# Kernel optimization log

Hardware: AMD Instinct MI355X
Metric: run time of the kernel (lower is better)

## Reference

```python
import jax, jax.numpy as jnp
import numpy as np

B = 256
# (Cin, Cout, K, Hout) for each of the 6 deformable conv layers; input is 33x33
_LAYERS = [(1, 16, 3, 31), (16, 32, 3, 29), (32, 16, 5, 25), (16, 16, 7, 19), (16, 8, 5, 15), (8, 4, 3, 13)]


def setup_inputs() -> dict:
    key = jax.random.key(0)
    ks = jax.random.split(key, 24)
    inp = {"x": jax.random.normal(ks[0], (B, 1, 33, 33), dtype=jnp.float32)}
    for i, (ci, co, k, ho) in enumerate(_LAYERS):
        inp[f"off{i+1}"] = jax.random.normal(ks[1 + i], (1, 2 * k * k, ho, ho), dtype=jnp.float32)
        inp[f"w{i+1}"] = jax.random.normal(ks[7 + i], (co, ci, k, k), dtype=jnp.float32) / float(np.sqrt(ci * k * k))
        inp[f"b{i+1}"] = jnp.zeros((co,), jnp.float32)
    inp["w7"] = jax.random.normal(ks[13], (13 * 13 * 4, 256), dtype=jnp.float32) / 26.0
    inp["b7"] = jnp.zeros((256,), jnp.float32)
    inp["w8"] = jax.random.normal(ks[14], (256, 10), dtype=jnp.float32) / 16.0
    inp["b8"] = jnp.zeros((10,), jnp.float32)
    inp["perm"] = jnp.arange(13 * 13, dtype=jnp.int32)  # fixed spatial permutation (perm_6.ordenar)
    return inp


def _deform_conv(x, offset, weight, bias):
    # torchvision DeformConv2d, stride=1, padding=0, fixed offsets shared across batch.
    Bn, Cin, H, W = x.shape
    Cout, _, K, _ = weight.shape
    Ho, Wo = offset.shape[-2], offset.shape[-1]
    K2 = K * K
    off = offset[0].reshape(K2, 2, Ho, Wo)  # channel layout: [2k]=dy, [2k+1]=dx
    ky, kx = jnp.meshgrid(jnp.arange(K), jnp.arange(K), indexing='ij')
    py = jnp.arange(Ho, dtype=x.dtype)[None, :, None] + ky.reshape(-1, 1, 1) + off[:, 0]  # [K2,Ho,Wo]
    px = jnp.arange(Wo, dtype=x.dtype)[None, None, :] + kx.reshape(-1, 1, 1) + off[:, 1]
    y0f = jnp.floor(py); x0f = jnp.floor(px)
    wy = py - y0f; wx = px - x0f
    y0 = y0f.astype(jnp.int32); x0 = x0f.astype(jnp.int32)
    xf = x.reshape(Bn, Cin, H * W)

    def gather(yi, xi):
        valid = ((yi >= 0) & (yi < H) & (xi >= 0) & (xi < W)).astype(x.dtype)
        idx = (jnp.clip(yi, 0, H - 1) * W + jnp.clip(xi, 0, W - 1)).reshape(-1)
        v = xf[:, :, idx].reshape(Bn, Cin, K2, Ho, Wo)
        return v * valid[None, None]

    s = (gather(y0, x0) * ((1 - wy) * (1 - wx))[None, None]
         + gather(y0, x0 + 1) * ((1 - wy) * wx)[None, None]
         + gather(y0 + 1, x0) * (wy * (1 - wx))[None, None]
         + gather(y0 + 1, x0 + 1) * (wy * wx)[None, None])  # [B,Cin,K2,Ho,Wo]
    out = jnp.einsum('bckhw,ock->bohw', s, weight.reshape(Cout, Cin, K2))
    return out + bias[None, :, None, None]


def reference(x, off1, off2, off3, off4, off5, off6,
              w1, b1, w2, b2, w3, b3, w4, b4, w5, b5, w6, b6,
              w7, b7, w8, b8, perm):
    offs = (off1, off2, off3, off4, off5, off6)
    ws = (w1, w2, w3, w4, w5, w6)
    bs = (b1, b2, b3, b4, b5, b6)
    for off, w, b in zip(offs, ws, bs):
        x = jax.nn.relu(_deform_conv(x, off, w, b))
    Bn = x.shape[0]
    x = x.reshape(Bn, 4, 13 * 13)[:, :, perm].reshape(Bn, -1)  # perm_6.ordenar as spatial permutation
    h = jax.nn.relu(x @ w7 + b7)
    return h @ w8 + b8
```

## Files before the change

### kernel.cpp

```cpp
#include <hip/hip_runtime.h>

struct WtArgs { const float* src[6]; int co[6], ci[6], k2[6], dstoff[6]; };

__global__ __launch_bounds__(256)
void transpose_weights(WtArgs a, float* __restrict__ dst0)
{
    const int L = blockIdx.x;
    const float* __restrict__ s = a.src[L];
    float* __restrict__ d = dst0 + a.dstoff[L];
    const int co = a.co[L], ci = a.ci[L], k2 = a.k2[L];
    const int n = co * ci * k2;
    for (int i = threadIdx.x; i < n; i += 256) {
        int k = i % k2;
        int c = (i / k2) % ci;
        int o = i / (k2 * ci);
        d[(k * ci + c) * co + o] = s[i];
    }
}

struct MetaArgs { const float* off[6]; int P[6], K[6], WO[6], H[6], W[6], base[6]; };

__global__ __launch_bounds__(256)
void build_meta(MetaArgs a, float* __restrict__ meta0)
{
    const int L = blockIdx.y;
    const float* __restrict__ off = a.off[L];
    const int P = a.P[L], K = a.K[L], WOv = a.WO[L], H = a.H[L], Wv = a.W[L];
    const int N = P * K * K;
    float* __restrict__ m = meta0 + (size_t)a.base[L] * 8;
    for (int e = blockIdx.x * 256 + threadIdx.x; e < N; e += gridDim.x * 256) {
        const int k = e / P, p = e - k * P;
        const int ho = p / WOv, wo = p - ho * WOv;
        const int ky = k / K, kx = k - ky * K;
        const float dy = off[(2 * k)     * P + p];
        const float dx = off[(2 * k + 1) * P + p];
        const float py = (float)(ho + ky) + dy;
        const float px = (float)(wo + kx) + dx;
        const float y0f = floorf(py), x0f = floorf(px);
        const float wy = py - y0f, wx = px - x0f;
        const int y0 = (int)y0f, x0 = (int)x0f;
        const int y1 = y0 + 1,  x1 = x0 + 1;
        const bool vy0 = ((unsigned)y0 < (unsigned)H);
        const bool vy1 = ((unsigned)y1 < (unsigned)H);
        const bool vx0 = ((unsigned)x0 < (unsigned)Wv);
        const bool vx1 = ((unsigned)x1 < (unsigned)Wv);
        const int cy0 = min(max(y0, 0), H - 1) * Wv;
        const int cy1 = min(max(y1, 0), H - 1) * Wv;
        const int cx0 = min(max(x0, 0), Wv - 1);
        const int cx1 = min(max(x1, 0), Wv - 1);
        int4 mi;
        mi.x = cy0 + cx0; mi.y = cy0 + cx1; mi.z = cy1 + cx0; mi.w = cy1 + cx1;
        float4 mw;
        mw.x = (vy0 && vx0) ? (1.f - wy) * (1.f - wx) : 0.f;
        mw.y = (vy0 && vx1) ? (1.f - wy) * wx         : 0.f;
        mw.z = (vy1 && vx0) ? wy * (1.f - wx)         : 0.f;
        mw.w = (vy1 && vx1) ? wy * wx                 : 0.f;
        *(int4*)(m + (size_t)e * 8)     = mi;
        *(float4*)(m + (size_t)e * 8 + 4) = mw;
    }
}

template<int CIN, int CINW, int COUT, int K, int H, int W, int HO, int WO,
         int S, int KSEG, int NT, int NCOMB, bool SPLITOUT, bool MET>
__global__ __launch_bounds__(NT)
void deform_lds(const float* __restrict__ x0, const float* __restrict__ x1,
                const float* __restrict__ off, const float* __restrict__ meta,
                const float* __restrict__ wT, const float* __restrict__ bias,
                float* __restrict__ y, size_t pstride)
{
    constexpr int K2 = K * K, HW = H * W, P = HO * WO;
    constexpr int PW = ((P + 63) / 64) * 64;
    constexpr int KLEN = (K2 + KSEG - 1) / KSEG;
    constexpr int PSTR = (COUT % 2 == 0) ? COUT + 1 : COUT;
    static_assert(NT >= KSEG * PW, "NT too small for KSEG*PW");

    __shared__ __align__(16) float simg[HW * S];
    __shared__ float part[(KSEG > 1) ? (KSEG - 1) * P * PSTR : 1];

    const int tid = threadIdx.x;
    const int b   = blockIdx.x;
    const int h   = SPLITOUT ? blockIdx.y : 0;

    const size_t xoff = (size_t)b * CINW * HW + (SPLITOUT ? (size_t)h * CIN * HW : 0);
    const float* xb  = x0 + xoff;
    const float* xb1 = (NCOMB == 2) ? (x1 + xoff) : nullptr;
    for (int i = tid; i < CIN * HW; i += NT) {
        int c = i / HW, hw = i - c * HW;
        float v;
        if constexpr (NCOMB == 2) v = fmaxf(xb[i] + xb1[i], 0.f);
        else                      v = xb[i];
        simg[hw * S + c] = v;
    }
    __syncthreads();

    const int g  = tid / PW;
    const int p  = tid - g * PW;
    const int pc = (p < P) ? p : (P - 1);
    const bool active = (p < P);

    float acc[COUT];
#pragma unroll
    for (int o = 0; o < COUT; ++o) acc[o] = 0.f;

    if (g < KSEG) {
        if (g == 0 && (!SPLITOUT || h == 0)) {
#pragma unroll
            for (int o = 0; o < COUT; ++o) acc[o] = bias[o];
        }
        const int ho = pc / WO, wo = pc - ho * WO;
        const int kb = g * KLEN;

        auto fma_block = [&](int i00, int i01, int i10, int i11,
                             float w00, float w01, float w10, float w11,
                             int kku) {
            const float* __restrict__ r00 = simg + i00 * S;
            const float* __restrict__ r01 = simg + i01 * S;
            const float* __restrict__ r10 = simg + i10 * S;
            const float* __restrict__ r11 = simg + i11 * S;
            const float* __restrict__ wk = wT + kku * (CINW * COUT)
                                         + (SPLITOUT ? h * (CIN * COUT) : 0);
            if constexpr (CIN % 4 == 0) {
#pragma unroll
                for (int c4 = 0; c4 < CIN / 4; ++c4) {
                    const float4 v00 = *(const float4*)(r00 + c4 * 4);
                    const float4 v01 = *(const float4*)(r01 + c4 * 4);
                    const float4 v10 = *(const float4*)(r10 + c4 * 4);
                    const float4 v11 = *(const float4*)(r11 + c4 * 4);
                    float4 sa;
                    sa.x = fmaf(w00, v00.x, fmaf(w01, v01.x, fmaf(w10, v10.x, w11 * v11.x)));
                    sa.y = fmaf(w00, v00.y, fmaf(w01, v01.y, fmaf(w10, v10.y, w11 * v11.y)));
                    sa.z = fmaf(w00, v00.z, fmaf(w01, v01.z, fmaf(w10, v10.z, w11 * v11.z)));
                    sa.w = fmaf(w00, v00.w, fmaf(w01, v01.w, fmaf(w10, v10.w, w11 * v11.w)));
                    const float* __restrict__ wc = wk + (c4 * 4) * COUT;
#pragma unroll
                    for (int o = 0; o < COUT; ++o) acc[o] = fmaf(wc[o], sa.x, acc[o]);
#pragma unroll
                    for (int o = 0; o < COUT; ++o) acc[o] = fmaf(wc[COUT + o], sa.y, acc[o]);
#pragma unroll
                    for (int o = 0; o < COUT; ++o) acc[o] = fmaf(wc[2 * COUT + o], sa.z, acc[o]);
#pragma unroll
                    for (int o = 0; o < COUT; ++o) acc[o] = fmaf(wc[3 * COUT + o], sa.w, acc[o]);
                }
            } else {
#pragma unroll
                for (int c = 0; c < CIN; ++c) {
                    float sa = fmaf(w00, r00[c], fmaf(w01, r01[c],
                               fmaf(w10, r10[c], w11 * r11[c])));
#pragma unroll
                    for (int o = 0; o < COUT; ++o)
                        acc[o] = fmaf(wk[c * COUT + o], sa, acc[o]);
                }
            }
        };

        if constexpr (MET) {
            const int kf = (kb < K2) ? kb : (K2 - 1);
            int4   nmi = *(const int4*)  (meta + (size_t)(kf * P + pc) * 8);
            float4 nmw = *(const float4*)(meta + (size_t)(kf * P + pc) * 8 + 4);

#pragma unroll 1
            for (int j = 0; j < KLEN; ++j) {
                const int k  = kb + j;
                const int kk = (k < K2) ? k : (K2 - 1);
                const int4   mi  = nmi;
                const float4 mwv = nmw;
                const int kn = (k + 1 < K2) ? (k + 1) : (K2 - 1);
                nmi = *(const int4*)  (meta + (size_t)(kn * P + pc) * 8);
                nmw = *(const float4*)(meta + (size_t)(kn * P + pc) * 8 + 4);

                float w00 = mwv.x, w01 = mwv.y, w10 = mwv.z, w11 = mwv.w;
                if constexpr (K2 % KSEG != 0) {
                    const float kv = (k < K2) ? 1.f : 0.f;
                    w00 *= kv; w01 *= kv; w10 *= kv; w11 *= kv;
                }
                const int kku = __builtin_amdgcn_readfirstlane(kk);
                fma_block(mi.x, mi.y, mi.z, mi.w, w00, w01, w10, w11, kku);
            }
        } else {
            const int kf = (kb < K2) ? kb : (K2 - 1);
            float ndy = off[(2 * kf)     * P + pc];
            float ndx = off[(2 * kf + 1) * P + pc];

#pragma unroll 1
            for (int j = 0; j < KLEN; ++j) {
                const int k  = kb + j;
                const int kk = (k < K2) ? k : (K2 - 1);
                const float dy = ndy, dx = ndx;
                const int kn = (k + 1 < K2) ? (k + 1) : (K2 - 1);
                ndy = off[(2 * kn)     * P + pc];
                ndx = off[(2 * kn + 1) * P + pc];

                const int ky = kk / K, kx = kk - ky * K;
                const float py = (float)(ho + ky) + dy;
                const float px = (float)(wo + kx) + dx;
                const float y0f = floorf(py), x0f = floorf(px);
                const float wy = py - y0f, wx = px - x0f;
                const int y0 = (int)y0f, x0 = (int)x0f;
                const int y1 = y0 + 1,  x1i = x0 + 1;
                const bool vy0 = ((unsigned)y0  < (unsigned)H);
                const bool vy1 = ((unsigned)y1  < (unsigned)H);
                const bool vx0 = ((unsigned)x0  < (unsigned)W);
                const bool vx1 = ((unsigned)x1i < (unsigned)W);
                const int cy0 = min(max(y0, 0), H - 1) * W;
                const int cy1 = min(max(y1, 0), H - 1) * W;
                const int cx0 = min(max(x0, 0), W - 1);
                const int cx1 = min(max(x1i, 0), W - 1);
                float w00 = (vy0 && vx0) ? (1.f - wy) * (1.f - wx) : 0.f;
                float w01 = (vy0 && vx1) ? (1.f - wy) * wx         : 0.f;
                float w10 = (vy1 && vx0) ? wy * (1.f - wx)         : 0.f;
                float w11 = (vy1 && vx1) ? wy * wx                 : 0.f;
                if constexpr (K2 % KSEG != 0) {
                    const float kv = (k < K2) ? 1.f : 0.f;
                    w00 *= kv; w01 *= kv; w10 *= kv; w11 *= kv;
                }
                const int kku = __builtin_amdgcn_readfirstlane(kk);
                fma_block(cy0 + cx0, cy0 + cx1, cy1 + cx0, cy1 + cx1,
                          w00, w01, w10, w11, kku);
            }
        }

        if (g > 0 && active) {
#pragma unroll
            for (int o = 0; o < COUT; ++o)
                part[(g - 1) * (P * PSTR) + p * PSTR + o] = acc[o];
        }
    }

    if constexpr (KSEG > 1) __syncthreads();

    if (g == 0 && active) {
        if constexpr (KSEG > 1) {
#pragma unroll
            for (int gg = 1; gg < KSEG; ++gg)
#pragma unroll
                for (int o = 0; o < COUT; ++o)
                    acc[o] += part[(gg - 1) * (P * PSTR) + p * PSTR + o];
        }
        float* yb = y + (SPLITOUT ? (size_t)h * pstride : 0) + (size_t)b * COUT * P;
#pragma unroll
        for (int o = 0; o < COUT; ++o)
            yb[o * P + p] = SPLITOUT ? acc[o] : fmaxf(acc[o], 0.f);
    }
}

__global__ __launch_bounds__(256)
void fc_head(const float* __restrict__ x6, const float* __restrict__ w7,
             const float* __restrict__ b7, const float* __restrict__ w8,
             const float* __restrict__ b8, const int* __restrict__ perm,
             float* __restrict__ out)
{
    constexpr int F = 676;
    __shared__ float sx[F];
    __shared__ float sh[256];

    const int tid = threadIdx.x;
    const int b   = blockIdx.x;

    for (int i = tid; i < F; i += 256) {
        int c = i / 169, p = i - c * 169;
        sx[i] = x6[(size_t)b * F + c * 169 + perm[p]];
    }
    __syncthreads();

    float acc = b7[tid];
#pragma unroll 4
    for (int i = 0; i < F; ++i)
        acc = fmaf(sx[i], w7[i * 256 + tid], acc);
    sh[tid] = fmaxf(acc, 0.f);
    __syncthreads();

    if (tid < 10) {
        float a = b8[tid];
#pragma unroll 8
        for (int j = 0; j < 256; ++j)
            a = fmaf(sh[j], w8[j * 10 + tid], a);
        out[(size_t)b * 10 + tid] = a;
    }
}

extern "C" void kernel_launch(void* const* d_in, const int* in_sizes, int n_in,
                              void* d_out, int out_size, void* d_ws, size_t ws_size,
                              hipStream_t stream)
{
    const float* x    = (const float*)d_in[0];
    const float* off1 = (const float*)d_in[1];
    const float* w1   = (const float*)d_in[2];
    const float* b1   = (const float*)d_in[3];
    const float* off2 = (const float*)d_in[4];
    const float* w2   = (const float*)d_in[5];
    const float* b2   = (const float*)d_in[6];
    const float* off3 = (const float*)d_in[7];
    const float* w3   = (const float*)d_in[8];
    const float* b3   = (const float*)d_in[9];
    const float* off4 = (const float*)d_in[10];
    const float* w4   = (const float*)d_in[11];
    const float* b4   = (const float*)d_in[12];
    const float* off5 = (const float*)d_in[13];
    const float* w5   = (const float*)d_in[14];
    const float* b5   = (const float*)d_in[15];
    const float* off6 = (const float*)d_in[16];
    const float* w6   = (const float*)d_in[17];
    const float* b6   = (const float*)d_in[18];
    const float* w7   = (const float*)d_in[19];
    const float* b7   = (const float*)d_in[20];
    const float* w8   = (const float*)d_in[21];
    const float* b8   = (const float*)d_in[22];
    const int*   perm = (const int*)d_in[23];
    float* out = (float*)d_out;

    const int woff[6] = {0, 144, 4752, 17552, 30096, 33296};
    float* ws   = (float*)d_ws;
    float* wt   = ws;
    float* buf0 = ws + 33792;
    float* buf1 = buf0 + 3936256;

    float* a1   = buf0;
    float* a2   = buf1;
    float* p1L2 = ws + 13419520;
    float* a3   = buf0;
    float* p1L3 = ws + 10859520;
    float* a4p0 = buf1;
    float* a4p1 = buf1 + 1478656;
    float* a5   = buf0;
    float* a6   = buf1;
    float* meta = ws + 20308992;

    const int mbase[6] = {0, 8649, 16218, 31843, 49532, 55157};
    const int MTOT = 56678;

    const bool splitL3 = (ws_size >= (size_t)13419520 * sizeof(float));
    const bool splitL2 = (ws_size >= (size_t)20308992 * sizeof(float));
    const bool metaOK  = (ws_size >= (size_t)(20308992 + MTOT * 8) * sizeof(float));
    const size_t pstrL3 = (size_t)(p1L3 - a3);
    const size_t pstrL2 = (size_t)(p1L2 - a2);
    const size_t pstrL4 = 1478656;

    WtArgs wa;
    wa.src[0] = w1; wa.src[1] = w2; wa.src[2] = w3;
    wa.src[3] = w4; wa.src[4] = w5; wa.src[5] = w6;
    const int cos[6] = {16, 32, 16, 16, 8, 4};
    const int cis[6] = {1, 16, 32, 16, 16, 8};
    const int k2s[6] = {9, 9, 25, 49, 25, 9};
    for (int i = 0; i < 6; ++i) {
        wa.co[i] = cos[i]; wa.ci[i] = cis[i];
        wa.k2[i] = k2s[i]; wa.dstoff[i] = woff[i];
    }
    transpose_weights<<<dim3(6), dim3(256), 0, stream>>>(wa, wt);

    const dim3 g1(256), g2(256, 2);

    if (metaOK) {
        MetaArgs ma;
        ma.off[0] = off1; ma.off[1] = off2; ma.off[2] = off3;
        ma.off[3] = off4; ma.off[4] = off5; ma.off[5] = off6;
        const int Ps[6]  = {961, 841, 625, 361, 225, 169};
        const int Ks[6]  = {3, 3, 5, 7, 5, 3};
        const int WOs[6] = {31, 29, 25, 19, 15, 13};
        const int Hs[6]  = {33, 31, 29, 25, 19, 15};
        const int Ws_[6] = {33, 31, 29, 25, 19, 15};
        for (int i = 0; i < 6; ++i) {
            ma.P[i] = Ps[i]; ma.K[i] = Ks[i]; ma.WO[i] = WOs[i];
            ma.H[i] = Hs[i]; ma.W[i] = Ws_[i]; ma.base[i] = mbase[i];
        }
        build_meta<<<dim3(64, 6), dim3(256), 0, stream>>>(ma, meta);

        deform_lds< 1,  1, 16, 3, 33, 33, 31, 31,  1, 1, 1024, 1, false, true>
            <<<g1, dim3(1024), 0, stream>>>(x, nullptr, off1, meta + (size_t)mbase[0]*8, wt + woff[0], b1, a1, 0);
        deform_lds< 8, 16, 32, 3, 31, 31, 29, 29, 12, 1,  896, 1, true,  true>
            <<<g2, dim3(896),  0, stream>>>(a1, nullptr, off2, meta + (size_t)mbase[1]*8, wt + woff[1], b2, a2, pstrL2);
        deform_lds<16, 32, 16, 5, 29, 29, 25, 25, 20, 1,  640, 2, true,  true>
            <<<g2, dim3(640),  0, stream>>>(a2, p1L2,   off3, meta + (size_t)mbase[2]*8, wt + woff[2], b3, a3, pstrL3);
        deform_lds< 8, 16, 16, 7, 25, 25, 19, 19, 12, 2,  768, 2, true,  true>
            <<<g2, dim3(768),  0, stream>>>(a3, p1L3,   off4, meta + (size_t)mbase[3]*8, wt + woff[3], b4, a4p0, pstrL4);
        deform_lds<16, 16,  8, 5, 19, 19, 15, 15, 20, 4, 1024, 2, false, true>
            <<<g1, dim3(1024), 0, stream>>>(a4p0, a4p1, off5, meta + (size_t)mbase[4]*8, wt + woff[4], b5, a5, 0);
        deform_lds< 8,  8,  4, 3, 15, 15, 13, 13, 12, 5,  960, 1, false, true>
            <<<g1, dim3(960),  0, stream>>>(a5, nullptr, off6, meta + (size_t)mbase[5]*8, wt + woff[5], b6, a6, 0);
    } else {
        deform_lds< 1,  1, 16, 3, 33, 33, 31, 31,  1, 1, 1024, 1, false, false>
            <<<g1, dim3(1024), 0, stream>>>(x, nullptr, off1, nullptr, wt + woff[0], b1, a1, 0);
        if (splitL2) {
            deform_lds< 8, 16, 32, 3, 31, 31, 29, 29, 12, 1, 1024, 1, true, false>
                <<<g2, dim3(1024), 0, stream>>>(a1, nullptr, off2, nullptr, wt + woff[1], b2, a2, pstrL2);
        } else {
            deform_lds<16, 16, 32, 3, 31, 31, 29, 29, 20, 1, 1024, 1, false, false>
                <<<g1, dim3(1024), 0, stream>>>(a1, nullptr, off2, nullptr, wt + woff[1], b2, a2, 0);
        }
        if (splitL3) {
            if (splitL2) {
                deform_lds<16, 32, 16, 5, 29, 29, 25, 25, 20, 1, 1024, 2, true, false>
                    <<<g2, dim3(1024), 0, stream>>>(a2, p1L2, off3, nullptr, wt + woff[2], b3, a3, pstrL3);
            } else {
                deform_lds<16, 32, 16, 5, 29, 29, 25, 25, 20, 1, 1024, 1, true, false>
                    <<<g2, dim3(1024), 0, stream>>>(a2, nullptr, off3, nullptr, wt + woff[2], b3, a3, pstrL3);
            }
            deform_lds< 8, 16, 16, 7, 25, 25, 19, 19, 12, 2,  768, 2, true, false>
                <<<g2, dim3(768),  0, stream>>>(a3, p1L3, off4, nullptr, wt + woff[3], b4, a4p0, pstrL4);
        } else {
            deform_lds<32, 32, 16, 5, 29, 29, 25, 25, 36, 1, 1024, 1, false, false>
                <<<g1, dim3(1024), 0, stream>>>(a2, nullptr, off3, nullptr, wt + woff[2], b3, a3, 0);
            deform_lds< 8, 16, 16, 7, 25, 25, 19, 19, 12, 2,  768, 1, true, false>
                <<<g2, dim3(768),  0, stream>>>(a3, nullptr, off4, nullptr, wt + woff[3], b4, a4p0, pstrL4);
        }
        deform_lds<16, 16,  8, 5, 19, 19, 15, 15, 20, 4, 1024, 2, false, false>
            <<<g1, dim3(1024), 0, stream>>>(a4p0, a4p1, off5, nullptr, wt + woff[4], b5, a5, 0);
        deform_lds< 8,  8,  4, 3, 15, 15, 13, 13, 12, 5,  960, 1, false, false>
            <<<g1, dim3(960),  0, stream>>>(a5, nullptr, off6, nullptr, wt + woff[5], b6, a6, 0);
    }

    fc_head<<<dim3(256), dim3(256), 0, stream>>>(a6, w7, b7, w8, b8, perm, out);
}
```

Before: 271.0 us.

## Split layer 3 input channels three ways and sum three partials in layer 4

Layer 3 now splits its 32 input channels across three blocks per image (12 channels each, the last chunk zero-padded) instead of two. Layer 4's load stage sums three partial outputs and applies ReLU. This raises block count and cuts per-block LDS and serial work for layer 3, at the cost of one more partial buffer to write and read and some wasted padded channels. The path is taken only when the workspace is large enough.

```diff
diff --git a/kernel.cpp b/kernel.cpp
--- a/kernel.cpp
+++ b/kernel.cpp
@@ -55,7 +55,7 @@
         mw.y = (vy0 && vx1) ? (1.f - wy) * wx         : 0.f;
         mw.z = (vy1 && vx0) ? wy * (1.f - wx)         : 0.f;
         mw.w = (vy1 && vx1) ? wy * wx                 : 0.f;
-        *(int4*)(m + (size_t)e * 8)     = mi;
+        *(int4*)(m + (size_t)e * 8)       = mi;
         *(float4*)(m + (size_t)e * 8 + 4) = mw;
     }
 }
@@ -64,9 +64,10 @@
          int S, int KSEG, int NT, int NCOMB, bool SPLITOUT, bool MET>
 __global__ __launch_bounds__(NT)
 void deform_lds(const float* __restrict__ x0, const float* __restrict__ x1,
-                const float* __restrict__ off, const float* __restrict__ meta,
-                const float* __restrict__ wT, const float* __restrict__ bias,
-                float* __restrict__ y, size_t pstride)
+                const float* __restrict__ x2, const float* __restrict__ off,
+                const float* __restrict__ meta, const float* __restrict__ wT,
+                const float* __restrict__ bias, float* __restrict__ y,
+                size_t pstride)
 {
     constexpr int K2 = K * K, HW = H * W, P = HO * WO;
     constexpr int PW = ((P + 63) / 64) * 64;
@@ -83,12 +84,19 @@
 
     const size_t xoff = (size_t)b * CINW * HW + (SPLITOUT ? (size_t)h * CIN * HW : 0);
     const float* xb  = x0 + xoff;
-    const float* xb1 = (NCOMB == 2) ? (x1 + xoff) : nullptr;
+    const float* xb1 = (NCOMB >= 2) ? (x1 + xoff) : nullptr;
+    const float* xb2 = (NCOMB == 3) ? (x2 + xoff) : nullptr;
     for (int i = tid; i < CIN * HW; i += NT) {
         int c = i / HW, hw = i - c * HW;
-        float v;
-        if constexpr (NCOMB == 2) v = fmaxf(xb[i] + xb1[i], 0.f);
-        else                      v = xb[i];
+        bool ok = true;
+        if constexpr (SPLITOUT) ok = (h * CIN + c < CINW);
+        float v = 0.f;
+        if (ok) {
+            v = xb[i];
+            if constexpr (NCOMB >= 2) v += xb1[i];
+            if constexpr (NCOMB == 3) v += xb2[i];
+            if constexpr (NCOMB >= 2) v = fmaxf(v, 0.f);
+        }
         simg[hw * S + c] = v;
     }
     __syncthreads();
@@ -331,7 +339,8 @@
     const bool splitL3 = (ws_size >= (size_t)13419520 * sizeof(float));
     const bool splitL2 = (ws_size >= (size_t)20308992 * sizeof(float));
     const bool metaOK  = (ws_size >= (size_t)(20308992 + MTOT * 8) * sizeof(float));
-    const size_t pstrL3 = (size_t)(p1L3 - a3);
+    const bool split3  = (ws_size >= (size_t)24245248 * sizeof(float));
+    const size_t X      = 10825728;
     const size_t pstrL2 = (size_t)(p1L2 - a2);
     const size_t pstrL4 = 1478656;
 
@@ -347,7 +356,7 @@
     }
     transpose_weights<<<dim3(6), dim3(256), 0, stream>>>(wa, wt);
 
-    const dim3 g1(256), g2(256, 2);
+    const dim3 g1(256), g2(256, 2), g3(256, 3);
 
     if (metaOK) {
         MetaArgs ma;
@@ -365,47 +374,56 @@
         build_meta<<<dim3(64, 6), dim3(256), 0, stream>>>(ma, meta);
 
         deform_lds< 1,  1, 16, 3, 33, 33, 31, 31,  1, 1, 1024, 1, false, true>
-            <<<g1, dim3(1024), 0, stream>>>(x, nullptr, off1, meta + (size_t)mbase[0]*8, wt + woff[0], b1, a1, 0);
+            <<<g1, dim3(1024), 0, stream>>>(x, nullptr, nullptr, off1, meta + (size_t)mbase[0]*8, wt + woff[0], b1, a1, 0);
         deform_lds< 8, 16, 32, 3, 31, 31, 29, 29, 12, 1,  896, 1, true,  true>
-            <<<g2, dim3(896),  0, stream>>>(a1, nullptr, off2, meta + (size_t)mbase[1]*8, wt + woff[1], b2, a2, pstrL2);
-        deform_lds<16, 32, 16, 5, 29, 29, 25, 25, 20, 1,  640, 2, true,  true>
-            <<<g2, dim3(640),  0, stream>>>(a2, p1L2,   off3, meta + (size_t)mbase[2]*8, wt + woff[2], b3, a3, pstrL3);
-        deform_lds< 8, 16, 16, 7, 25, 25, 19, 19, 12, 2,  768, 2, true,  true>
-            <<<g2, dim3(768),  0, stream>>>(a3, p1L3,   off4, meta + (size_t)mbase[3]*8, wt + woff[3], b4, a4p0, pstrL4);
+            <<<g2, dim3(896),  0, stream>>>(a1, nullptr, nullptr, off2, meta + (size_t)mbase[1]*8, wt + woff[1], b2, a2, pstrL2);
+
+        if (split3) {
+            deform_lds<12, 32, 16, 5, 29, 29, 25, 25, 12, 1,  640, 2, true,  true>
+                <<<g3, dim3(640),  0, stream>>>(a2, p1L2, nullptr, off3, meta + (size_t)mbase[2]*8, wt + woff[2], b3, a3, X);
+            deform_lds< 8, 16, 16, 7, 25, 25, 19, 19, 12, 2,  768, 3, true,  true>
+                <<<g2, dim3(768),  0, stream>>>(a3, a3 + X, a3 + 2 * X, off4, meta + (size_t)mbase[3]*8, wt + woff[3], b4, a4p0, pstrL4);
+        } else {
+            deform_lds<16, 32, 16, 5, 29, 29, 25, 25, 20, 1,  640, 2, true,  true>
+                <<<g2, dim3(640),  0, stream>>>(a2, p1L2, nullptr, off3, meta + (size_t)mbase[2]*8, wt + woff[2], b3, a3, X);
+            deform_lds< 8, 16, 16, 7, 25, 25, 19, 19, 12, 2,  768, 2, true,  true>
+                <<<g2, dim3(768),  0, stream>>>(a3, a3 + X, nullptr, off4, meta + (size_t)mbase[3]*8, wt + woff[3], b4, a4p0, pstrL4);
+        }
+
         deform_lds<16, 16,  8, 5, 19, 19, 15, 15, 20, 4, 1024, 2, false, true>
-            <<<g1, dim3(1024), 0, stream>>>(a4p0, a4p1, off5, meta + (size_t)mbase[4]*8, wt + woff[4], b5, a5, 0);
+            <<<g1, dim3(1024), 0, stream>>>(a4p0, a4p1, nullptr, off5, meta + (size_t)mbase[4]*8, wt + woff[4], b5, a5, 0);
         deform_lds< 8,  8,  4, 3, 15, 15, 13, 13, 12, 5,  960, 1, false, true>
-            <<<g1, dim3(960),  0, stream>>>(a5, nullptr, off6, meta + (size_t)mbase[5]*8, wt + woff[5], b6, a6, 0);
+            <<<g1, dim3(960),  0, stream>>>(a5, nullptr, nullptr, off6, meta + (size_t)mbase[5]*8, wt + woff[5], b6, a6, 0);
     } else {
         deform_lds< 1,  1, 16, 3, 33, 33, 31, 31,  1, 1, 1024, 1, false, false>
-            <<<g1, dim3(1024), 0, stream>>>(x, nullptr, off1, nullptr, wt + woff[0], b1, a1, 0);
+            <<<g1, dim3(1024), 0, stream>>>(x, nullptr, nullptr, off1, nullptr, wt + woff[0], b1, a1, 0);
         if (splitL2) {
             deform_lds< 8, 16, 32, 3, 31, 31, 29, 29, 12, 1, 1024, 1, true, false>
-                <<<g2, dim3(1024), 0, stream>>>(a1, nullptr, off2, nullptr, wt + woff[1], b2, a2, pstrL2);
+                <<<g2, dim3(1024), 0, stream>>>(a1, nullptr, nullptr, off2, nullptr, wt + woff[1], b2, a2, pstrL2);
         } else {
             deform_lds<16, 16, 32, 3, 31, 31, 29, 29, 20, 1, 1024, 1, false, false>
-                <<<g1, dim3(1024), 0, stream>>>(a1, nullptr, off2, nullptr, wt + woff[1], b2, a2, 0);
+                <<<g1, dim3(1024), 0, stream>>>(a1, nullptr, nullptr, off2, nullptr, wt + woff[1], b2, a2, 0);
         }
         if (splitL3) {
             if (splitL2) {
                 deform_lds<16, 32, 16, 5, 29, 29, 25, 25, 20, 1, 1024, 2, true, false>
-                    <<<g2, dim3(1024), 0, stream>>>(a2, p1L2, off3, nullptr, wt + woff[2], b3, a3, pstrL3);
+                    <<<g2, dim3(1024), 0, stream>>>(a2, p1L2, nullptr, off3, nullptr, wt + woff[2], b3, a3, X);
             } else {
                 deform_lds<16, 32, 16, 5, 29, 29, 25, 25, 20, 1, 1024, 1, true, false>
-                    <<<g2, dim3(1024), 0, stream>>>(a2, nullptr, off3, nullptr, wt + woff[2], b3, a3, pstrL3);
+                    <<<g2, dim3(1024), 0, stream>>>(a2, nullptr, nullptr, off3, nullptr, wt + woff[2], b3, a3, X);
             }
             deform_lds< 8, 16, 16, 7, 25, 25, 19, 19, 12, 2,  768, 2, true, false>
-                <<<g2, dim3(768),  0, stream>>>(a3, p1L3, off4, nullptr, wt + woff[3], b4, a4p0, pstrL4);
+                <<<g2, dim3(768),  0, stream>>>(a3, a3 + X, nullptr, off4, nullptr, wt + woff[3], b4, a4p0, pstrL4);
         } else {
             deform_lds<32, 32, 16, 5, 29, 29, 25, 25, 36, 1, 1024, 1, false, false>
-                <<<g1, dim3(1024), 0, stream>>>(a2, nullptr, off3, nullptr, wt + woff[2], b3, a3, 0);
+                <<<g1, dim3(1024), 0, stream>>>(a2, nullptr, nullptr, off3, nullptr, wt + woff[2], b3, a3, 0);
             deform_lds< 8, 16, 16, 7, 25, 25, 19, 19, 12, 2,  768, 1, true, false>
-                <<<g2, dim3(768),  0, stream>>>(a3, nullptr, off4, nullptr, wt + woff[3], b4, a4p0, pstrL4);
+                <<<g2, dim3(768),  0, stream>>>(a3, nullptr, nullptr, off4, nullptr, wt + woff[3], b4, a4p0, pstrL4);
         }
         deform_lds<16, 16,  8, 5, 19, 19, 15, 15, 20, 4, 1024, 2, false, false>
-            <<<g1, dim3(1024), 0, stream>>>(a4p0, a4p1, off5, nullptr, wt + woff[4], b5, a5, 0);
+            <<<g1, dim3(1024), 0, stream>>>(a4p0, a4p1, nullptr, off5, nullptr, wt + woff[4], b5, a5, 0);
         deform_lds< 8,  8,  4, 3, 15, 15, 13, 13, 12, 5,  960, 1, false, false>
-            <<<g1, dim3(960),  0, stream>>>(a5, nullptr, off6, nullptr, wt + woff[5], b6, a6, 0);
+            <<<g1, dim3(960),  0, stream>>>(a5, nullptr, nullptr, off6, nullptr, wt + woff[5], b6, a6, 0);
     }
 
     fc_head<<<dim3(256), dim3(256), 0, stream>>>(a6, w7, b7, w8, b8, perm, out);
```

Result: no change. 268.9 us (-0.8%).
